# Performance work log

Hardware: AMD Instinct MI355X
Metric: run time of the kernel (lower is better)

Reference implementation:

```python
import jax, jax.numpy as jnp
import numpy as np

B, N, C, H, W = 16, 8, 3, 48, 48
K = 5          # kernel_size=[5]
NK = 4         # hardcoded multi-kernel weight groups in the module


def setup_inputs() -> dict:
    key = jax.random.key(0)
    k1, k2, k3 = jax.random.split(key, 3)
    frames = jax.random.normal(k1, (B, N, C, H, W), jnp.float32)
    # core as produced by _convert_dict: [B, N, K*K, 3, 4, H, W]
    core = jax.random.normal(k2, (B, N, K * K, C, NK, H, W), jnp.float32)
    kernel_weight = jax.random.normal(k3, (B, N, NK, C, H, W), jnp.float32)
    return {"frames": frames, "core": core, "kernel_weight": kernel_weight}


def reference(frames, core, kernel_weight):
    b, n, c, h, w = frames.shape
    kk = K * K
    # torch: padded_kernel = stack([core[5]], dim=2) -> [B,N,1,25,3,4,H,W]
    #        .view(B, N, 4, -1, 3, 48, 48): row-major reinterpretation of the
    #        flattened (25*3*4)=300 middle dims into (4, 25, 3).
    pk = core.reshape(b, n, NK, kk, c, h, w)
    # kernel_weight.unsqueeze(3) -> [B,N,4,1,3,H,W]; mean over the 4 groups
    wk = jnp.mean(pk * kernel_weight[:, :, :, None], axis=2)  # [B,N,25,3,H,W]
    # im2col-style gather: pad by K//2 and stack the 25 spatial shifts
    p = K // 2
    fp = jnp.pad(frames, ((0, 0), (0, 0), (0, 0), (p, p), (p, p)))
    img_stack = jnp.stack(
        [fp[..., i:i + h, j:j + w] for i in range(K) for j in range(K)],
        axis=2,
    )  # [B,N,25,3,H,W]
    # pred_rgb[i] = sum_k sum_c wk[:,:,k,i] * img_stack[:,:,k,c]
    frames_sum = jnp.sum(img_stack, axis=3)  # [B,N,25,H,W]
    pred_img_i = jnp.einsum('bnkihw,bnkhw->bnihw', wk, frames_sum)  # [B,N,3,H,W]
    pred_img = jnp.mean(pred_img_i, axis=1)  # [B,3,H,W]
    return pred_img_i, pred_img
```

## Files before the change

kernel.cpp:

```cpp
#include <hip/hip_runtime.h>
#include <stdint.h>
#include <stddef.h>

constexpr int B_ = 16, N_ = 8, C_ = 3, H_ = 48, W_ = 48, K_ = 5, NK_ = 4;
constexpr int HW_ = H_ * W_;
constexpr int IMGS_ = B_ * N_;
constexpr int PW_ = W_ + 4;
constexpr int PH_ = H_ + 4;
constexpr int PHW_ = PH_ * PW_;
constexpr int QPI_ = HW_ / 4;

typedef float f32x4 __attribute__((ext_vector_type(4)));

__global__ void kcs(const float* __restrict__ frames, float* __restrict__ cs) {
    int id = blockIdx.x * blockDim.x + threadIdx.x;
    if (id >= IMGS_ * PHW_) return;
    int img = id / PHW_;
    int rem = id - img * PHW_;
    int ph = rem / PW_;
    int pw = rem - ph * PW_;
    int h = ph - 2, w = pw - 2;
    float s = 0.f;
    if ((unsigned)h < (unsigned)H_ && (unsigned)w < (unsigned)W_) {
        const float* f = frames + (size_t)img * (C_ * HW_) + h * W_ + w;
        s = f[0] + f[HW_] + f[2 * HW_];
    }
    cs[id] = s;
}

__global__ __launch_bounds__(64) void kmain(const float* __restrict__ core,
                                            const float* __restrict__ kw,
                                            const float* __restrict__ cs,
                                            float* __restrict__ out) {
    int tid = blockIdx.x * 64 + threadIdx.x;
    int img = tid / QPI_;
    int r = tid - img * QPI_;
    int h = r / (W_ / 4);
    int q = r - h * (W_ / 4);
    int w0 = q * 4;
    int pix0 = h * W_ + w0;

    float fs[5][8];
    const float* csp = cs + img * PHW_ + h * PW_ + w0;
#pragma unroll
    for (int rr = 0; rr < 5; ++rr) {
        f32x4 a = *(const f32x4*)(csp + rr * PW_);
        f32x4 b = *(const f32x4*)(csp + rr * PW_ + 4);
        fs[rr][0] = a.x; fs[rr][1] = a.y; fs[rr][2] = a.z; fs[rr][3] = a.w;
        fs[rr][4] = b.x; fs[rr][5] = b.y; fs[rr][6] = b.z; fs[rr][7] = b.w;
    }

    const float* cp = core + (size_t)img * (300 * HW_) + pix0;
    const float* kp = kw + (size_t)img * (12 * HW_) + pix0;

    float p[3][4] = {};
    for (int g = 0; g < 4; ++g) {
#pragma unroll
        for (int c = 0; c < 3; ++c) {
            float t[4] = {0.f, 0.f, 0.f, 0.f};
            const float* cpk = cp + (size_t)(g * 75 + c) * HW_;
#pragma unroll
            for (int k = 0; k < 25; ++k) {
                f32x4 d = __builtin_nontemporal_load(
                    (const f32x4*)(cpk + (size_t)(k * 3) * HW_));
                int di = k / 5, dj = k - di * 5;
                t[0] += d.x * fs[di][dj + 0];
                t[1] += d.y * fs[di][dj + 1];
                t[2] += d.z * fs[di][dj + 2];
                t[3] += d.w * fs[di][dj + 3];
            }
            f32x4 kd = __builtin_nontemporal_load(
                (const f32x4*)(kp + (size_t)(g * 3 + c) * HW_));
            p[c][0] += kd.x * t[0];
            p[c][1] += kd.y * t[1];
            p[c][2] += kd.z * t[2];
            p[c][3] += kd.w * t[3];
        }
    }

    float* op = out + (size_t)img * (3 * HW_) + pix0;
#pragma unroll
    for (int c = 0; c < 3; ++c) {
        f32x4 v = {0.25f * p[c][0], 0.25f * p[c][1], 0.25f * p[c][2], 0.25f * p[c][3]};
        *(f32x4*)(op + (size_t)c * HW_) = v;
    }
}

__global__ void kmean(const float* __restrict__ outi, float* __restrict__ outm) {
    int id = blockIdx.x * blockDim.x + threadIdx.x;
    if (id >= B_ * 3 * HW_) return;
    int b = id / (3 * HW_);
    int rem = id - b * (3 * HW_);
    const float* p = outi + (size_t)b * (N_ * 3 * HW_) + rem;
    float s = 0.f;
#pragma unroll
    for (int n = 0; n < N_; ++n) s += p[(size_t)n * 3 * HW_];
    outm[id] = s * 0.125f;
}

extern "C" void kernel_launch(void* const* d_in, const int* in_sizes, int n_in,
                              void* d_out, int out_size, void* d_ws, size_t ws_size,
                              hipStream_t stream) {
    const float* frames = (const float*)d_in[0];
    const float* core = (const float*)d_in[1];
    const float* kw = (const float*)d_in[2];
    float* cs = (float*)d_ws;
    float* outi = (float*)d_out;
    float* outm = outi + (size_t)B_ * N_ * 3 * HW_;

    kcs<<<(IMGS_ * PHW_ + 255) / 256, 256, 0, stream>>>(frames, cs);
    kmain<<<IMGS_ * QPI_ / 64, 64, 0, stream>>>(core, kw, cs, outi);
    kmean<<<(B_ * 3 * HW_ + 255) / 256, 256, 0, stream>>>(outi, outm);
}
```

Baseline: 532.5 us.

## Split NK weight groups across warps and reduce partial sums in shared memory

Each 256-thread block now covers 256 pixels of one image, with each of four 64-lane wavefronts handling one of the four kernel-weight groups instead of one thread looping over all groups. Partial products go to shared memory and are reduced after a barrier, which gives four times as many threads and more memory-level parallelism for streaming the large core tensor. Nontemporal loads are replaced with plain loads. The cost is duplicated frame-sum loads per group, 12 KB of LDS per block, and a sync-plus-reduction step.

```diff
diff --git a/kernel.cpp b/kernel.cpp
--- a/kernel.cpp
+++ b/kernel.cpp
@@ -8,7 +8,7 @@
 constexpr int PW_ = W_ + 4;
 constexpr int PH_ = H_ + 4;
 constexpr int PHW_ = PH_ * PW_;
-constexpr int QPI_ = HW_ / 4;
+constexpr int CHUNKS_ = HW_ / 256;
 
 typedef float f32x4 __attribute__((ext_vector_type(4)));
 
@@ -28,17 +28,20 @@
     cs[id] = s;
 }
 
-__global__ __launch_bounds__(64) void kmain(const float* __restrict__ core,
-                                            const float* __restrict__ kw,
-                                            const float* __restrict__ cs,
-                                            float* __restrict__ out) {
-    int tid = blockIdx.x * 64 + threadIdx.x;
-    int img = tid / QPI_;
-    int r = tid - img * QPI_;
-    int h = r / (W_ / 4);
-    int q = r - h * (W_ / 4);
-    int w0 = q * 4;
-    int pix0 = h * W_ + w0;
+__global__ __launch_bounds__(256) void kmain(const float* __restrict__ core,
+                                             const float* __restrict__ kw,
+                                             const float* __restrict__ cs,
+                                             float* __restrict__ out) {
+    __shared__ float red[12 * 4 * 64];
+
+    int t = threadIdx.x;
+    int q = t & 63;
+    int g = t >> 6;
+    int img = blockIdx.x / CHUNKS_;
+    int chunk = blockIdx.x - img * CHUNKS_;
+    int pix0 = chunk * 256 + q * 4;
+    int h = pix0 / W_;
+    int w0 = pix0 - h * W_;
 
     float fs[5][8];
     const float* csp = cs + img * PHW_ + h * PW_ + w0;
@@ -50,39 +53,43 @@
         fs[rr][4] = b.x; fs[rr][5] = b.y; fs[rr][6] = b.z; fs[rr][7] = b.w;
     }
 
-    const float* cp = core + (size_t)img * (300 * HW_) + pix0;
-    const float* kp = kw + (size_t)img * (12 * HW_) + pix0;
+    const float* cp = core + (size_t)img * (300 * HW_) + (size_t)(g * 75) * HW_ + pix0;
+    const float* kp = kw + (size_t)img * (12 * HW_) + (size_t)(g * 3) * HW_ + pix0;
 
-    float p[3][4] = {};
-    for (int g = 0; g < 4; ++g) {
 #pragma unroll
-        for (int c = 0; c < 3; ++c) {
-            float t[4] = {0.f, 0.f, 0.f, 0.f};
-            const float* cpk = cp + (size_t)(g * 75 + c) * HW_;
+    for (int c = 0; c < 3; ++c) {
+        float t0 = 0.f, t1 = 0.f, t2 = 0.f, t3 = 0.f;
 #pragma unroll
-            for (int k = 0; k < 25; ++k) {
-                f32x4 d = __builtin_nontemporal_load(
-                    (const f32x4*)(cpk + (size_t)(k * 3) * HW_));
-                int di = k / 5, dj = k - di * 5;
-                t[0] += d.x * fs[di][dj + 0];
-                t[1] += d.y * fs[di][dj + 1];
-                t[2] += d.z * fs[di][dj + 2];
-                t[3] += d.w * fs[di][dj + 3];
-            }
-            f32x4 kd = __builtin_nontemporal_load(
-                (const f32x4*)(kp + (size_t)(g * 3 + c) * HW_));
-            p[c][0] += kd.x * t[0];
-            p[c][1] += kd.y * t[1];
-            p[c][2] += kd.z * t[2];
-            p[c][3] += kd.w * t[3];
+        for (int k = 0; k < 25; ++k) {
+            f32x4 d = *(const f32x4*)(cp + (size_t)(k * 3 + c) * HW_);
+            int di = k / 5, dj = k - di * 5;
+            t0 += d.x * fs[di][dj + 0];
+            t1 += d.y * fs[di][dj + 1];
+            t2 += d.z * fs[di][dj + 2];
+            t3 += d.w * fs[di][dj + 3];
         }
+        f32x4 kd = *(const f32x4*)(kp + (size_t)c * HW_);
+        int base = ((g * 3 + c) * 4) * 64 + q;
+        red[base + 0 * 64] = kd.x * t0;
+        red[base + 1 * 64] = kd.y * t1;
+        red[base + 2 * 64] = kd.z * t2;
+        red[base + 3 * 64] = kd.w * t3;
     }
 
-    float* op = out + (size_t)img * (3 * HW_) + pix0;
+    __syncthreads();
+
+    if (t < 192) {
+        int c = t >> 6;
+        int qq = t & 63;
+        f32x4 o;
 #pragma unroll
-    for (int c = 0; c < 3; ++c) {
-        f32x4 v = {0.25f * p[c][0], 0.25f * p[c][1], 0.25f * p[c][2], 0.25f * p[c][3]};
-        *(f32x4*)(op + (size_t)c * HW_) = v;
+        for (int j = 0; j < 4; ++j) {
+            int base = (c * 4 + j) * 64 + qq;
+            float s = red[base] + red[base + 3 * 4 * 64]
+                    + red[base + 6 * 4 * 64] + red[base + 9 * 4 * 64];
+            o[j] = 0.25f * s;
+        }
+        *(f32x4*)(out + (size_t)img * (3 * HW_) + (size_t)c * HW_ + chunk * 256 + qq * 4) = o;
     }
 }
 
@@ -109,6 +116,6 @@
     float* outm = outi + (size_t)B_ * N_ * 3 * HW_;
 
     kcs<<<(IMGS_ * PHW_ + 255) / 256, 256, 0, stream>>>(frames, cs);
-    kmain<<<IMGS_ * QPI_ / 64, 64, 0, stream>>>(core, kw, cs, outi);
+    kmain<<<IMGS_ * CHUNKS_, 256, 0, stream>>>(core, kw, cs, outi);
     kmean<<<(B_ * 3 * HW_ + 255) / 256, 256, 0, stream>>>(outi, outm);
 }
```

New measurement: 482.7 us, median of 2. -9.3%, faster.
